# Kernel optimization log

Hardware: AMD Instinct MI355X
Metric: run time of the kernel (lower is better)

## Reference

```python
import jax, jax.numpy as jnp
import numpy as np

N_NODES = 50000
N_HYPEREDGES = 50000
E = 320000
D = 256


def _prelu(x, a):
    return jnp.where(x >= 0, x, a * x)


def _hypergraph_conv(x, hei, W, b, num_nodes, num_edges):
    # PyG HypergraphConv, use_attention=False, heads=1:
    # out = D^{-1} H B^{-1} H^T (X W^T) + b
    src = hei[0]  # node indices, [E]
    he = hei[1]   # hyperedge indices, [E]
    xw = x @ W.T  # [N, D] node transform (lin has no bias)
    ones = jnp.ones((hei.shape[1],), x.dtype)
    deg_n = jax.ops.segment_sum(ones, src, num_segments=num_nodes)   # node degree D
    deg_e = jax.ops.segment_sum(ones, he, num_segments=num_edges)    # hyperedge size B
    d_inv = jnp.where(deg_n > 0, 1.0 / deg_n, 0.0)
    b_inv = jnp.where(deg_e > 0, 1.0 / deg_e, 0.0)
    # node -> hyperedge aggregation, scaled by B^{-1}
    edge_feat = b_inv[:, None] * jax.ops.segment_sum(xw[src], he, num_segments=num_edges)  # [n_he, D]
    # hyperedge -> node aggregation, scaled by D^{-1}
    out = d_inv[:, None] * jax.ops.segment_sum(edge_feat[he], src, num_segments=num_nodes)  # [N, D]
    return out + b


def setup_inputs() -> dict:
    key = jax.random.key(0)
    ks = jax.random.split(key, 6)
    std = np.sqrt(2.0 / D)  # kaiming_normal
    x = jax.random.normal(ks[0], (N_NODES, D), dtype=jnp.float32)
    hyper_edge_index = jax.random.randint(ks[1], (2, E), 0, N_HYPEREDGES, dtype=jnp.int64)
    W1 = jax.random.normal(ks[2], (D, D), dtype=jnp.float32) * std
    b1 = jnp.zeros((D,), jnp.float32)
    W2 = jax.random.normal(ks[3], (D, D), dtype=jnp.float32) * std
    b2 = jnp.zeros((D,), jnp.float32)
    prelu_a = jnp.asarray(0.25, jnp.float32)
    return {"x": x, "W1": W1, "b1": b1, "W2": W2, "b2": b2,
            "prelu_a": prelu_a, "hyper_edge_index": hyper_edge_index}


def reference(x, W1, b1, W2, b2, prelu_a, hyper_edge_index):
    out = _hypergraph_conv(x, hyper_edge_index, W1, b1, N_NODES, N_HYPEREDGES)
    out = _prelu(out, prelu_a)
    out = _hypergraph_conv(out, hyper_edge_index, W2, b2, N_NODES, N_HYPEREDGES)
    out = out + x  # residual
    out = _prelu(out, prelu_a)
    return out
```

## Files before the change

### kernel.cpp

```cpp
#include <hip/hip_runtime.h>

#define NN    50000
#define NHE   50000
#define NEDGE 320000
#define DD    256

#define SB    1024
#define NBLK  ((NN + SB - 1) / SB)

typedef float f32x4 __attribute__((ext_vector_type(4)));
typedef short short8 __attribute__((ext_vector_type(8)));

static __device__ __forceinline__ unsigned short f2b(float f) {
    union { float f; unsigned u; } c; c.f = f;
    unsigned u = c.u;
    u += 0x7fffu + ((u >> 16) & 1u);
    return (unsigned short)(u >> 16);
}
static __device__ __forceinline__ float b2f_lo(unsigned v) {
    union { unsigned u; float f; } c; c.u = v << 16; return c.f;
}
static __device__ __forceinline__ float b2f_hi(unsigned v) {
    union { unsigned u; float f; } c; c.u = v & 0xffff0000u; return c.f;
}
static __device__ __forceinline__ unsigned pack2(float a, float b) {
    return (unsigned)f2b(a) | ((unsigned)f2b(b) << 16);
}

static __device__ __forceinline__ void glds16(const unsigned short* g, unsigned short* l) {
    __builtin_amdgcn_global_load_lds((const __attribute__((address_space(1))) unsigned int*)g,
                                     (__attribute__((address_space(3))) unsigned int*)l,
                                     16, 0, 0);
}

__global__ __launch_bounds__(256) void k_count(const int* __restrict__ src,
                                               const int* __restrict__ he,
                                               int* __restrict__ cnt_n,
                                               int* __restrict__ cnt_e,
                                               int* __restrict__ rank_n,
                                               int* __restrict__ rank_e) {
    int t  = blockIdx.x * 256 + threadIdx.x;
    int e0 = t * 4;
    if (e0 >= NEDGE) return;
    int4 s = *(const int4*)(src + e0);
    int4 h = *(const int4*)(he + e0);
    int4 rn, re;
    rn.x = atomicAdd(&cnt_n[s.x], 1);
    rn.y = atomicAdd(&cnt_n[s.y], 1);
    rn.z = atomicAdd(&cnt_n[s.z], 1);
    rn.w = atomicAdd(&cnt_n[s.w], 1);
    re.x = atomicAdd(&cnt_e[h.x], 1);
    re.y = atomicAdd(&cnt_e[h.y], 1);
    re.z = atomicAdd(&cnt_e[h.z], 1);
    re.w = atomicAdd(&cnt_e[h.w], 1);
    *(int4*)(rank_n + e0) = rn;
    *(int4*)(rank_e + e0) = re;
}

__global__ __launch_bounds__(256) void k_scan_a(const int* __restrict__ cnt_n,
                                                const int* __restrict__ cnt_e,
                                                int* __restrict__ bsum,
                                                const float* __restrict__ w1,
                                                const float* __restrict__ w2,
                                                unsigned short* __restrict__ o1,
                                                unsigned short* __restrict__ o2) {
    int b = blockIdx.x;
    if (b >= 2 * NBLK) {
        int t = (b - 2 * NBLK) * 256 + threadIdx.x;
        const int n4 = DD * DD / 4;
        const float* s = (t < n4) ? w1 : w2;
        unsigned short* d = (t < n4) ? o1 : o2;
        int i = (t < n4) ? t : t - n4;
        float4 v = ((const float4*)s)[i];
        uint2 o;
        o.x = pack2(v.x, v.y);
        o.y = pack2(v.z, v.w);
        ((uint2*)d)[i] = o;
        return;
    }
    int seg = b / NBLK, lb = b % NBLK;
    const int* cnt = seg ? cnt_e : cnt_n;
    int t = threadIdx.x;
    int idx = lb * SB + t * 4;
    int s = 0;
#pragma unroll
    for (int j = 0; j < 4; ++j)
        if (idx + j < NN) s += cnt[idx + j];
    __shared__ int red[256];
    red[t] = s;
    __syncthreads();
    for (int o = 128; o > 0; o >>= 1) {
        if (t < o) red[t] += red[t + o];
        __syncthreads();
    }
    if (t == 0) bsum[b] = red[0];
}

__global__ __launch_bounds__(64) void k_scan_b(const int* __restrict__ bsum,
                                               int* __restrict__ bbase) {
    if (threadIdx.x == 0) {
        int r = 0;
        for (int i = 0; i < NBLK; ++i) { bbase[i] = r; r += bsum[i]; }
        bbase[2 * NBLK] = r;
        r = 0;
        for (int i = NBLK; i < 2 * NBLK; ++i) { bbase[i] = r; r += bsum[i]; }
        bbase[2 * NBLK + 1] = r;
    }
}

__global__ __launch_bounds__(256) void k_scan_c(const int* __restrict__ cnt_n,
                                                const int* __restrict__ cnt_e,
                                                const int* __restrict__ bbase,
                                                int* __restrict__ off_n,
                                                int* __restrict__ off_e) {
    int b   = blockIdx.x;
    int seg = b / NBLK, lb = b % NBLK;
    const int* cnt = seg ? cnt_e : cnt_n;
    int* off = seg ? off_e : off_n;
    int t = threadIdx.x;
    int idx = lb * SB + t * 4;
    int v[4];
    int tsum = 0;
#pragma unroll
    for (int j = 0; j < 4; ++j) {
        v[j] = (idx + j < NN) ? cnt[idx + j] : 0;
        tsum += v[j];
    }
    __shared__ int sc[256];
    sc[t] = tsum;
    __syncthreads();
    for (int o = 1; o < 256; o <<= 1) {
        int val = (t >= o) ? sc[t - o] : 0;
        __syncthreads();
        sc[t] += val;
        __syncthreads();
    }
    int p = bbase[b] + sc[t] - tsum;
#pragma unroll
    for (int j = 0; j < 4; ++j) {
        if (idx + j < NN) off[idx + j] = p;
        p += v[j];
    }
    if (b == 0 && t == 0) off_n[NN] = bbase[2 * NBLK];
    if (b == NBLK && t == 0) off_e[NHE] = bbase[2 * NBLK + 1];
}

__global__ __launch_bounds__(256) void k_fill(const int* __restrict__ src,
                                              const int* __restrict__ he,
                                              const int* __restrict__ off_n,
                                              const int* __restrict__ off_e,
                                              const int* __restrict__ rank_n,
                                              const int* __restrict__ rank_e,
                                              int* __restrict__ adj_n,
                                              int* __restrict__ adj_e) {
    int t  = blockIdx.x * 256 + threadIdx.x;
    int e0 = t * 4;
    if (e0 >= NEDGE) return;
    int4 s  = *(const int4*)(src + e0);
    int4 h  = *(const int4*)(he + e0);
    int4 rn = *(const int4*)(rank_n + e0);
    int4 re = *(const int4*)(rank_e + e0);
    int on0 = off_n[s.x], on1 = off_n[s.y], on2 = off_n[s.z], on3 = off_n[s.w];
    int oe0 = off_e[h.x], oe1 = off_e[h.y], oe2 = off_e[h.z], oe3 = off_e[h.w];
    adj_n[on0 + rn.x] = h.x;
    adj_n[on1 + rn.y] = h.y;
    adj_n[on2 + rn.z] = h.z;
    adj_n[on3 + rn.w] = h.w;
    adj_e[oe0 + re.x] = s.x;
    adj_e[oe1 + re.y] = s.y;
    adj_e[oe2 + re.z] = s.z;
    adj_e[oe3 + re.w] = s.w;
}

template <bool A32>
__global__ __launch_bounds__(256) void k_gemm128(const void* __restrict__ Av,
                                                 const unsigned short* __restrict__ Wb,
                                                 unsigned short* __restrict__ Cb, int M) {
    __shared__ __align__(16) unsigned short As[128 * 32];
    __shared__ __align__(16) unsigned short Bs[128 * 32];
    const int t    = threadIdx.x;
    const int m0   = blockIdx.x * 128;
    const int n0   = blockIdx.y * 128;
    const int lane = t & 63;
    const int wave = t >> 6;
    const int wm   = (wave >> 1) * 64;
    const int wn   = (wave & 1) * 64;
    const int fr   = lane & 15;
    const int fq   = lane >> 4;

    f32x4 acc[4][4] = {};

    const int rl0 = wave * 32 + (lane >> 2);
    const int ar = t >> 1;
    const int ah = t & 1;

    for (int k0 = 0; k0 < DD; k0 += 32) {
        __syncthreads();
#pragma unroll
        for (int q = 0; q < 2; ++q) {
            int rl = rl0 + q * 16;
            int c  = (lane & 3) ^ (rl & 3);
            glds16(Wb + (size_t)(n0 + rl) * DD + k0 + c * 8,
                   Bs + (size_t)(wave * 32 + q * 16) * 32);
        }
        if (A32) {
            int gr = m0 + ar; if (gr >= M) gr = M - 1;
            const float* p = (const float*)Av + (size_t)gr * DD + k0 + ah * 16;
            float4 f0 = ((const float4*)p)[0];
            float4 f1 = ((const float4*)p)[1];
            float4 f2 = ((const float4*)p)[2];
            float4 f3 = ((const float4*)p)[3];
            uint4 u0, u1;
            u0.x = pack2(f0.x, f0.y); u0.y = pack2(f0.z, f0.w);
            u0.z = pack2(f1.x, f1.y); u0.w = pack2(f1.z, f1.w);
            u1.x = pack2(f2.x, f2.y); u1.y = pack2(f2.z, f2.w);
            u1.z = pack2(f3.x, f3.y); u1.w = pack2(f3.z, f3.w);
            int p0 = (2 * ah) ^ (ar & 3);
            int p1 = (2 * ah + 1) ^ (ar & 3);
            *(uint4*)(As + ar * 32 + p0 * 8) = u0;
            *(uint4*)(As + ar * 32 + p1 * 8) = u1;
        } else {
#pragma unroll
            for (int q = 0; q < 2; ++q) {
                int rl = rl0 + q * 16;
                int gr = m0 + rl; if (gr >= M) gr = M - 1;
                int c  = (lane & 3) ^ (rl & 3);
                glds16((const unsigned short*)Av + (size_t)gr * DD + k0 + c * 8,
                       As + (size_t)(wave * 32 + q * 16) * 32);
            }
        }
        __syncthreads();

        short8 af[4], bf[4];
#pragma unroll
        for (int mt = 0; mt < 4; ++mt) {
            int r = wm + mt * 16 + fr;
            af[mt] = *(const short8*)(As + r * 32 + ((fq ^ (r & 3)) * 8));
        }
#pragma unroll
        for (int nt = 0; nt < 4; ++nt) {
            int r = wn + nt * 16 + fr;
            bf[nt] = *(const short8*)(Bs + r * 32 + ((fq ^ (r & 3)) * 8));
        }
#pragma unroll
        for (int mt = 0; mt < 4; ++mt)
#pragma unroll
            for (int nt = 0; nt < 4; ++nt)
                acc[mt][nt] = __builtin_amdgcn_mfma_f32_16x16x32_bf16(af[mt], bf[nt],
                                                                      acc[mt][nt], 0, 0, 0);
    }

#pragma unroll
    for (int mt = 0; mt < 4; ++mt) {
#pragma unroll
        for (int i = 0; i < 4; ++i) {
            int gm = m0 + wm + mt * 16 + fq * 4 + i;
            if (gm >= M) continue;
#pragma unroll
            for (int nt = 0; nt < 4; ++nt) {
                int gn = n0 + wn + nt * 16 + fr;
                Cb[(size_t)gm * DD + gn] = f2b(acc[mt][nt][i]);
            }
        }
    }
}

static __device__ __forceinline__ void acc8(float* a, uint4 v) {
    a[0] += b2f_lo(v.x); a[1] += b2f_hi(v.x);
    a[2] += b2f_lo(v.y); a[3] += b2f_hi(v.y);
    a[4] += b2f_lo(v.z); a[5] += b2f_hi(v.z);
    a[6] += b2f_lo(v.w); a[7] += b2f_hi(v.w);
}
static __device__ __forceinline__ void gather8(const unsigned short* __restrict__ srcb,
                                               const int* __restrict__ adj,
                                               int b, int e, int sl, float* a) {
#pragma unroll
    for (int i = 0; i < 8; ++i) a[i] = 0.f;
    for (int i = b; i < e; i += 8) {
        int g0 = adj[i];
        int g[8];
        g[0] = g0;
#pragma unroll
        for (int j = 1; j < 8; ++j) g[j] = (i + j < e) ? adj[i + j] : g0;
        uint4 v[8];
#pragma unroll
        for (int j = 0; j < 8; ++j)
            v[j] = *(const uint4*)(srcb + (size_t)g[j] * DD + sl * 8);
        acc8(a, v[0]);
#pragma unroll
        for (int j = 1; j < 8; ++j)
            if (i + j < e) acc8(a, v[j]);
    }
}

__global__ __launch_bounds__(256) void k_gather_edge_b(const unsigned short* __restrict__ xw,
                                                       unsigned short* __restrict__ ef,
                                                       const int* __restrict__ off,
                                                       const int* __restrict__ adj) {
    int tid = blockIdx.x * 256 + threadIdx.x;
    int w = tid >> 5;
    int sl = tid & 31;
    if (w >= NHE) return;
    int b = off[w], e = off[w + 1];
    float a[8];
    gather8(xw, adj, b, e, sl, a);
    float sc = (e > b) ? 1.f / (float)(e - b) : 0.f;
    uint4 o;
    o.x = pack2(a[0] * sc, a[1] * sc);
    o.y = pack2(a[2] * sc, a[3] * sc);
    o.z = pack2(a[4] * sc, a[5] * sc);
    o.w = pack2(a[6] * sc, a[7] * sc);
    *(uint4*)(ef + (size_t)w * DD + sl * 8) = o;
}

__global__ __launch_bounds__(256) void k_gather_node_mid_b(const unsigned short* __restrict__ ef,
                                                           unsigned short* __restrict__ h,
                                                           const int* __restrict__ off,
                                                           const int* __restrict__ adj,
                                                           const float* __restrict__ bias,
                                                           const float* __restrict__ aP) {
    int tid = blockIdx.x * 256 + threadIdx.x;
    int w = tid >> 5;
    int sl = tid & 31;
    if (w >= NN) return;
    int b = off[w], e = off[w + 1];
    float a[8];
    gather8(ef, adj, b, e, sl, a);
    float sc = (e > b) ? 1.f / (float)(e - b) : 0.f;
    float al = *aP;
    float4 bb0 = ((const float4*)bias)[sl * 2];
    float4 bb1 = ((const float4*)bias)[sl * 2 + 1];
    float r[8];
    r[0] = a[0] * sc + bb0.x; r[1] = a[1] * sc + bb0.y;
    r[2] = a[2] * sc + bb0.z; r[3] = a[3] * sc + bb0.w;
    r[4] = a[4] * sc + bb1.x; r[5] = a[5] * sc + bb1.y;
    r[6] = a[6] * sc + bb1.z; r[7] = a[7] * sc + bb1.w;
#pragma unroll
    for (int i = 0; i < 8; ++i) r[i] = (r[i] >= 0.f) ? r[i] : al * r[i];
    uint4 o;
    o.x = pack2(r[0], r[1]);
    o.y = pack2(r[2], r[3]);
    o.z = pack2(r[4], r[5]);
    o.w = pack2(r[6], r[7]);
    *(uint4*)(h + (size_t)w * DD + sl * 8) = o;
}

__global__ __launch_bounds__(256) void k_gather_node_final_b(const unsigned short* __restrict__ ef,
                                                             const float* __restrict__ x,
                                                             float* __restrict__ out,
                                                             const int* __restrict__ off,
                                                             const int* __restrict__ adj,
                                                             const float* __restrict__ bias,
                                                             const float* __restrict__ aP) {
    int tid = blockIdx.x * 256 + threadIdx.x;
    int w = tid >> 5;
    int sl = tid & 31;
    if (w >= NN) return;
    int b = off[w], e = off[w + 1];
    float a[8];
    gather8(ef, adj, b, e, sl, a);
    float sc = (e > b) ? 1.f / (float)(e - b) : 0.f;
    float al = *aP;
    float4 bb0 = ((const float4*)bias)[sl * 2];
    float4 bb1 = ((const float4*)bias)[sl * 2 + 1];
    const float* xp = x + (size_t)w * DD + sl * 8;
    float4 xv0 = *(const float4*)xp;
    float4 xv1 = *(const float4*)(xp + 4);
    float r[8];
    r[0] = a[0] * sc + bb0.x + xv0.x; r[1] = a[1] * sc + bb0.y + xv0.y;
    r[2] = a[2] * sc + bb0.z + xv0.z; r[3] = a[3] * sc + bb0.w + xv0.w;
    r[4] = a[4] * sc + bb1.x + xv1.x; r[5] = a[5] * sc + bb1.y + xv1.y;
    r[6] = a[6] * sc + bb1.z + xv1.z; r[7] = a[7] * sc + bb1.w + xv1.w;
#pragma unroll
    for (int i = 0; i < 8; ++i) r[i] = (r[i] >= 0.f) ? r[i] : al * r[i];
    float* op = out + (size_t)w * DD + sl * 8;
    *(float4*)op = make_float4(r[0], r[1], r[2], r[3]);
    *(float4*)(op + 4) = make_float4(r[4], r[5], r[6], r[7]);
}

extern "C" void kernel_launch(void* const* d_in, const int* in_sizes, int n_in,
                              void* d_out, int out_size, void* d_ws, size_t ws_size,
                              hipStream_t stream) {
    const float* x       = (const float*)d_in[0];
    const float* W1      = (const float*)d_in[1];
    const float* b1      = (const float*)d_in[2];
    const float* W2      = (const float*)d_in[3];
    const float* b2      = (const float*)d_in[4];
    const float* prelu_a = (const float*)d_in[5];
    const int*   hei     = (const int*)d_in[6];
    const int* idx_src = hei;
    const int* idx_he  = hei + NEDGE;

    float* out = (float*)d_out;
    unsigned short* B1 = (unsigned short*)d_ws;
    unsigned short* B2 = B1 + (size_t)NN * DD;
    int* off_n  = (int*)(B2 + (size_t)NN * DD);
    int* off_e  = off_n + NN + 1;
    int* cnt_n  = off_e + NHE + 1;
    int* cnt_e  = cnt_n + NN;
    int* adj_n  = cnt_e + NHE;
    int* adj_e  = adj_n + NEDGE;
    int* rank_n = adj_e + NEDGE;
    int* rank_e = rank_n + NEDGE;
    int* bsum   = rank_e + NEDGE;
    int* bbase  = bsum + 2 * NBLK;
    unsigned short* w1b = (unsigned short*)d_out;
    unsigned short* w2b = w1b + DD * DD;

    const int e4blocks = (NEDGE / 4 + 255) / 256;
    const int gblocks = (NN * 32 + 255) / 256;
    dim3 ggrid((NN + 127) / 128, DD / 128);

    hipMemsetAsync(cnt_n, 0, sizeof(int) * (NN + NHE), stream);
    k_count<<<e4blocks, 256, 0, stream>>>(idx_src, idx_he, cnt_n, cnt_e,
                                          rank_n, rank_e);
    k_scan_a<<<2 * NBLK + 128, 256, 0, stream>>>(cnt_n, cnt_e, bsum,
                                                 W1, W2, w1b, w2b);
    k_scan_b<<<1, 64, 0, stream>>>(bsum, bbase);
    k_scan_c<<<2 * NBLK, 256, 0, stream>>>(cnt_n, cnt_e, bbase, off_n, off_e);
    k_fill<<<e4blocks, 256, 0, stream>>>(idx_src, idx_he, off_n, off_e,
                                         rank_n, rank_e, adj_n, adj_e);

    k_gemm128<true><<<ggrid, 256, 0, stream>>>((const void*)x, w1b, B1, NN);
    k_gather_edge_b<<<gblocks, 256, 0, stream>>>(B1, B2, off_e, adj_e);
    k_gather_node_mid_b<<<gblocks, 256, 0, stream>>>(B2, B1, off_n, adj_n, b1, prelu_a);

    k_gemm128<false><<<ggrid, 256, 0, stream>>>((const void*)B1, w2b, B2, NN);
    k_gather_edge_b<<<gblocks, 256, 0, stream>>>(B2, B1, off_e, adj_e);
    k_gather_node_final_b<<<gblocks, 256, 0, stream>>>(B1, x, out, off_n, adj_n, b2, prelu_a);
}
```

Measured before the change: 308.9 us.

## Merge setup kernels, fold scan_b into scan_c, remap gathers to two rows per wave

Moves the weight bf16 conversion into the count kernel and drops the single-thread scan_b kernel by having each scan_c block compute its own base from the block sums. Runs the CSR fill and the first GEMM as one launch through block-index dispatch. Changes the gather kernels so each 64-lane wave processes two rows with 8-byte loads per lane and interleaved neighbor fetches, instead of one row per 32 lanes with 16-byte loads. This cuts launch count and serial gaps. The fused fill+GEMM has no dependency between its parts, but the per-block serial prefix and the narrower loads may add cost.

```diff
diff --git a/kernel.cpp b/kernel.cpp
--- a/kernel.cpp
+++ b/kernel.cpp
@@ -7,6 +7,7 @@
 
 #define SB    1024
 #define NBLK  ((NN + SB - 1) / SB)
+#define CNTB  ((NEDGE / 4 + 255) / 256)
 
 typedef float f32x4 __attribute__((ext_vector_type(4)));
 typedef short short8 __attribute__((ext_vector_type(8)));
@@ -33,13 +34,31 @@
                                      16, 0, 0);
 }
 
-__global__ __launch_bounds__(256) void k_count(const int* __restrict__ src,
-                                               const int* __restrict__ he,
-                                               int* __restrict__ cnt_n,
-                                               int* __restrict__ cnt_e,
-                                               int* __restrict__ rank_n,
-                                               int* __restrict__ rank_e) {
-    int t  = blockIdx.x * 256 + threadIdx.x;
+__global__ __launch_bounds__(256) void k_count_cvt(const int* __restrict__ src,
+                                                   const int* __restrict__ he,
+                                                   int* __restrict__ cnt_n,
+                                                   int* __restrict__ cnt_e,
+                                                   int* __restrict__ rank_n,
+                                                   int* __restrict__ rank_e,
+                                                   const float* __restrict__ w1,
+                                                   const float* __restrict__ w2,
+                                                   unsigned short* __restrict__ o1,
+                                                   unsigned short* __restrict__ o2) {
+    int bx = blockIdx.x;
+    if (bx >= CNTB) {
+        int t = (bx - CNTB) * 256 + threadIdx.x;
+        const int n4 = DD * DD / 4;
+        const float* s = (t < n4) ? w1 : w2;
+        unsigned short* d = (t < n4) ? o1 : o2;
+        int i = (t < n4) ? t : t - n4;
+        float4 v = ((const float4*)s)[i];
+        uint2 o;
+        o.x = pack2(v.x, v.y);
+        o.y = pack2(v.z, v.w);
+        ((uint2*)d)[i] = o;
+        return;
+    }
+    int t  = bx * 256 + threadIdx.x;
     int e0 = t * 4;
     if (e0 >= NEDGE) return;
     int4 s = *(const int4*)(src + e0);
@@ -59,25 +78,8 @@
 
 __global__ __launch_bounds__(256) void k_scan_a(const int* __restrict__ cnt_n,
                                                 const int* __restrict__ cnt_e,
-                                                int* __restrict__ bsum,
-                                                const float* __restrict__ w1,
-                                                const float* __restrict__ w2,
-                                                unsigned short* __restrict__ o1,
-                                                unsigned short* __restrict__ o2) {
-    int b = blockIdx.x;
-    if (b >= 2 * NBLK) {
-        int t = (b - 2 * NBLK) * 256 + threadIdx.x;
-        const int n4 = DD * DD / 4;
-        const float* s = (t < n4) ? w1 : w2;
-        unsigned short* d = (t < n4) ? o1 : o2;
-        int i = (t < n4) ? t : t - n4;
-        float4 v = ((const float4*)s)[i];
-        uint2 o;
-        o.x = pack2(v.x, v.y);
-        o.y = pack2(v.z, v.w);
-        ((uint2*)d)[i] = o;
-        return;
-    }
+                                                int* __restrict__ bsum) {
+    int b   = blockIdx.x;
     int seg = b / NBLK, lb = b % NBLK;
     const int* cnt = seg ? cnt_e : cnt_n;
     int t = threadIdx.x;
@@ -96,21 +98,9 @@
     if (t == 0) bsum[b] = red[0];
 }
 
-__global__ __launch_bounds__(64) void k_scan_b(const int* __restrict__ bsum,
-                                               int* __restrict__ bbase) {
-    if (threadIdx.x == 0) {
-        int r = 0;
-        for (int i = 0; i < NBLK; ++i) { bbase[i] = r; r += bsum[i]; }
-        bbase[2 * NBLK] = r;
-        r = 0;
-        for (int i = NBLK; i < 2 * NBLK; ++i) { bbase[i] = r; r += bsum[i]; }
-        bbase[2 * NBLK + 1] = r;
-    }
-}
-
 __global__ __launch_bounds__(256) void k_scan_c(const int* __restrict__ cnt_n,
                                                 const int* __restrict__ cnt_e,
-                                                const int* __restrict__ bbase,
+                                                const int* __restrict__ bsum,
                                                 int* __restrict__ off_n,
                                                 int* __restrict__ off_e) {
     int b   = blockIdx.x;
@@ -118,6 +108,15 @@
     const int* cnt = seg ? cnt_e : cnt_n;
     int* off = seg ? off_e : off_n;
     int t = threadIdx.x;
+    __shared__ int sb[NBLK];
+    __shared__ int binfo[2];
+    if (t < NBLK) sb[t] = bsum[seg * NBLK + t];
+    __syncthreads();
+    if (t == 0) {
+        int base = 0, tot = 0;
+        for (int j = 0; j < NBLK; ++j) { if (j < lb) base += sb[j]; tot += sb[j]; }
+        binfo[0] = base; binfo[1] = tot;
+    }
     int idx = lb * SB + t * 4;
     int v[4];
     int tsum = 0;
@@ -135,52 +134,24 @@
         sc[t] += val;
         __syncthreads();
     }
-    int p = bbase[b] + sc[t] - tsum;
+    int p = binfo[0] + sc[t] - tsum;
 #pragma unroll
     for (int j = 0; j < 4; ++j) {
         if (idx + j < NN) off[idx + j] = p;
         p += v[j];
     }
-    if (b == 0 && t == 0) off_n[NN] = bbase[2 * NBLK];
-    if (b == NBLK && t == 0) off_e[NHE] = bbase[2 * NBLK + 1];
-}
-
-__global__ __launch_bounds__(256) void k_fill(const int* __restrict__ src,
-                                              const int* __restrict__ he,
-                                              const int* __restrict__ off_n,
-                                              const int* __restrict__ off_e,
-                                              const int* __restrict__ rank_n,
-                                              const int* __restrict__ rank_e,
-                                              int* __restrict__ adj_n,
-                                              int* __restrict__ adj_e) {
-    int t  = blockIdx.x * 256 + threadIdx.x;
-    int e0 = t * 4;
-    if (e0 >= NEDGE) return;
-    int4 s  = *(const int4*)(src + e0);
-    int4 h  = *(const int4*)(he + e0);
-    int4 rn = *(const int4*)(rank_n + e0);
-    int4 re = *(const int4*)(rank_e + e0);
-    int on0 = off_n[s.x], on1 = off_n[s.y], on2 = off_n[s.z], on3 = off_n[s.w];
-    int oe0 = off_e[h.x], oe1 = off_e[h.y], oe2 = off_e[h.z], oe3 = off_e[h.w];
-    adj_n[on0 + rn.x] = h.x;
-    adj_n[on1 + rn.y] = h.y;
-    adj_n[on2 + rn.z] = h.z;
-    adj_n[on3 + rn.w] = h.w;
-    adj_e[oe0 + re.x] = s.x;
-    adj_e[oe1 + re.y] = s.y;
-    adj_e[oe2 + re.z] = s.z;
-    adj_e[oe3 + re.w] = s.w;
+    if (b == 0 && t == 0) off_n[NN] = binfo[1];
+    if (b == NBLK && t == 0) off_e[NHE] = binfo[1];
 }
 
 template <bool A32>
-__global__ __launch_bounds__(256) void k_gemm128(const void* __restrict__ Av,
-                                                 const unsigned short* __restrict__ Wb,
-                                                 unsigned short* __restrict__ Cb, int M) {
+static __device__ __forceinline__ void gemm128_body(const void* __restrict__ Av,
+                                                    const unsigned short* __restrict__ Wb,
+                                                    unsigned short* __restrict__ Cb,
+                                                    int M, int m0, int n0) {
     __shared__ __align__(16) unsigned short As[128 * 32];
     __shared__ __align__(16) unsigned short Bs[128 * 32];
     const int t    = threadIdx.x;
-    const int m0   = blockIdx.x * 128;
-    const int n0   = blockIdx.y * 128;
     const int lane = t & 63;
     const int wave = t >> 6;
     const int wm   = (wave >> 1) * 64;
@@ -265,117 +236,187 @@
     }
 }
 
-static __device__ __forceinline__ void acc8(float* a, uint4 v) {
+__global__ __launch_bounds__(256) void k_fill_gemm1(const int* __restrict__ src,
+                                                    const int* __restrict__ he,
+                                                    const int* __restrict__ off_n,
+                                                    const int* __restrict__ off_e,
+                                                    const int* __restrict__ rank_n,
+                                                    const int* __restrict__ rank_e,
+                                                    int* __restrict__ adj_n,
+                                                    int* __restrict__ adj_e,
+                                                    const float* __restrict__ x,
+                                                    const unsigned short* __restrict__ w1b,
+                                                    unsigned short* __restrict__ B1) {
+    int bx = blockIdx.x;
+    if (bx < CNTB) {
+        int t  = bx * 256 + threadIdx.x;
+        int e0 = t * 4;
+        if (e0 >= NEDGE) return;
+        int4 s  = *(const int4*)(src + e0);
+        int4 h  = *(const int4*)(he + e0);
+        int4 rn = *(const int4*)(rank_n + e0);
+        int4 re = *(const int4*)(rank_e + e0);
+        int on0 = off_n[s.x], on1 = off_n[s.y], on2 = off_n[s.z], on3 = off_n[s.w];
+        int oe0 = off_e[h.x], oe1 = off_e[h.y], oe2 = off_e[h.z], oe3 = off_e[h.w];
+        adj_n[on0 + rn.x] = h.x;
+        adj_n[on1 + rn.y] = h.y;
+        adj_n[on2 + rn.z] = h.z;
+        adj_n[on3 + rn.w] = h.w;
+        adj_e[oe0 + re.x] = s.x;
+        adj_e[oe1 + re.y] = s.y;
+        adj_e[oe2 + re.z] = s.z;
+        adj_e[oe3 + re.w] = s.w;
+        return;
+    }
+    int id = bx - CNTB;
+    int nt = id & 1, mt = id >> 1;
+    gemm128_body<true>((const void*)x, w1b, B1, NN, mt * 128, nt * 128);
+}
+
+__global__ __launch_bounds__(256) void k_gemm2(const unsigned short* __restrict__ Av,
+                                               const unsigned short* __restrict__ Wb,
+                                               unsigned short* __restrict__ Cb) {
+    gemm128_body<false>((const void*)Av, Wb, Cb, NN, blockIdx.y * 128, blockIdx.x * 128);
+}
+
+static __device__ __forceinline__ void acc4(float* a, uint2 v) {
     a[0] += b2f_lo(v.x); a[1] += b2f_hi(v.x);
     a[2] += b2f_lo(v.y); a[3] += b2f_hi(v.y);
-    a[4] += b2f_lo(v.z); a[5] += b2f_hi(v.z);
-    a[6] += b2f_lo(v.w); a[7] += b2f_hi(v.w);
-}
-static __device__ __forceinline__ void gather8(const unsigned short* __restrict__ srcb,
+}
+static __device__ __forceinline__ void gather2(const unsigned short* __restrict__ srcb,
                                                const int* __restrict__ adj,
-                                               int b, int e, int sl, float* a) {
-#pragma unroll
-    for (int i = 0; i < 8; ++i) a[i] = 0.f;
-    for (int i = b; i < e; i += 8) {
-        int g0 = adj[i];
-        int g[8];
-        g[0] = g0;
-#pragma unroll
-        for (int j = 1; j < 8; ++j) g[j] = (i + j < e) ? adj[i + j] : g0;
-        uint4 v[8];
-#pragma unroll
-        for (int j = 0; j < 8; ++j)
-            v[j] = *(const uint4*)(srcb + (size_t)g[j] * DD + sl * 8);
-        acc8(a, v[0]);
-#pragma unroll
-        for (int j = 1; j < 8; ++j)
-            if (i + j < e) acc8(a, v[j]);
-    }
-}
-
-__global__ __launch_bounds__(256) void k_gather_edge_b(const unsigned short* __restrict__ xw,
-                                                       unsigned short* __restrict__ ef,
-                                                       const int* __restrict__ off,
-                                                       const int* __restrict__ adj) {
+                                               int b0, int e0, int b1, int e1,
+                                               int ln, float* a0, float* a1) {
+#pragma unroll
+    for (int i = 0; i < 4; ++i) { a0[i] = 0.f; a1[i] = 0.f; }
+    int i0 = b0, i1 = b1;
+    while (i0 < e0 || i1 < e1) {
+        uint2 v0[8], v1[8];
+        bool act0 = i0 < e0, act1 = i1 < e1;
+        if (act0) {
+            int gg = adj[i0];
+            int g[8];
+            g[0] = gg;
+#pragma unroll
+            for (int j = 1; j < 8; ++j) g[j] = (i0 + j < e0) ? adj[i0 + j] : gg;
+#pragma unroll
+            for (int j = 0; j < 8; ++j)
+                v0[j] = *(const uint2*)(srcb + (size_t)g[j] * DD + ln * 4);
+        }
+        if (act1) {
+            int gg = adj[i1];
+            int g[8];
+            g[0] = gg;
+#pragma unroll
+            for (int j = 1; j < 8; ++j) g[j] = (i1 + j < e1) ? adj[i1 + j] : gg;
+#pragma unroll
+            for (int j = 0; j < 8; ++j)
+                v1[j] = *(const uint2*)(srcb + (size_t)g[j] * DD + ln * 4);
+        }
+        if (act0) {
+            acc4(a0, v0[0]);
+#pragma unroll
+            for (int j = 1; j < 8; ++j)
+                if (i0 + j < e0) acc4(a0, v0[j]);
+        }
+        if (act1) {
+            acc4(a1, v1[0]);
+#pragma unroll
+            for (int j = 1; j < 8; ++j)
+                if (i1 + j < e1) acc4(a1, v1[j]);
+        }
+        i0 += 8; i1 += 8;
+    }
+}
+
+__global__ __launch_bounds__(256) void k_gather_edge2(const unsigned short* __restrict__ xw,
+                                                      unsigned short* __restrict__ ef,
+                                                      const int* __restrict__ off,
+                                                      const int* __restrict__ adj) {
     int tid = blockIdx.x * 256 + threadIdx.x;
-    int w = tid >> 5;
-    int sl = tid & 31;
-    if (w >= NHE) return;
-    int b = off[w], e = off[w + 1];
-    float a[8];
-    gather8(xw, adj, b, e, sl, a);
-    float sc = (e > b) ? 1.f / (float)(e - b) : 0.f;
-    uint4 o;
-    o.x = pack2(a[0] * sc, a[1] * sc);
-    o.y = pack2(a[2] * sc, a[3] * sc);
-    o.z = pack2(a[4] * sc, a[5] * sc);
-    o.w = pack2(a[6] * sc, a[7] * sc);
-    *(uint4*)(ef + (size_t)w * DD + sl * 8) = o;
-}
-
-__global__ __launch_bounds__(256) void k_gather_node_mid_b(const unsigned short* __restrict__ ef,
-                                                           unsigned short* __restrict__ h,
-                                                           const int* __restrict__ off,
-                                                           const int* __restrict__ adj,
-                                                           const float* __restrict__ bias,
-                                                           const float* __restrict__ aP) {
+    int wv = tid >> 6;
+    int ln = tid & 63;
+    int r0 = wv * 2, r1 = r0 + 1;
+    if (r0 >= NHE) return;
+    int b0 = off[r0], e0 = off[r0 + 1];
+    int b1 = off[r1], e1 = off[r1 + 1];
+    float a0[4], a1[4];
+    gather2(xw, adj, b0, e0, b1, e1, ln, a0, a1);
+    float s0 = (e0 > b0) ? 1.f / (float)(e0 - b0) : 0.f;
+    float s1 = (e1 > b1) ? 1.f / (float)(e1 - b1) : 0.f;
+    uint2 o0, o1;
+    o0.x = pack2(a0[0] * s0, a0[1] * s0);
+    o0.y = pack2(a0[2] * s0, a0[3] * s0);
+    o1.x = pack2(a1[0] * s1, a1[1] * s1);
+    o1.y = pack2(a1[2] * s1, a1[3] * s1);
+    *(uint2*)(ef + (size_t)r0 * DD + ln * 4) = o0;
+    *(uint2*)(ef + (size_t)r1 * DD + ln * 4) = o1;
+}
+
+__global__ __launch_bounds__(256) void k_gather_node_mid2(const unsigned short* __restrict__ ef,
+                                                          unsigned short* __restrict__ h,
+                                                          const int* __restrict__ off,
+                                                          const int* __restrict__ adj,
+                                                          const float* __restrict__ bias,
+                                                          const float* __restrict__ aP) {
     int tid = blockIdx.x * 256 + threadIdx.x;
-    int w = tid >> 5;
-    int sl = tid & 31;
-    if (w >= NN) return;
-    int b = off[w], e = off[w + 1];
-    float a[8];
-    gather8(ef, adj, b, e, sl, a);
-    float sc = (e > b) ? 1.f / (float)(e - b) : 0.f;
+    int wv = tid >> 6;
+    int ln = tid & 63;
+    int r0 = wv * 2, r1 = r0 + 1;
+    if (r0 >= NN) return;
+    int b0 = off[r0], e0 = off[r0 + 1];
+    int b1 = off[r1], e1 = off[r1 + 1];
+    float a0[4], a1[4];
+    gather2(ef, adj, b0, e0, b1, e1, ln, a0, a1);
+    float s0 = (e0 > b0) ? 1.f / (float)(e0 - b0) : 0.f;
+    float s1 = (e1 > b1) ? 1.f / (float)(e1 - b1) : 0.f;
     float al = *aP;
-    float4 bb0 = ((const float4*)bias)[sl * 2];
-    float4 bb1 = ((const float4*)bias)[sl * 2 + 1];
+    float4 bb = ((const float4*)bias)[ln];
     float r[8];
-    r[0] = a[0] * sc + bb0.x; r[1] = a[1] * sc + bb0.y;
-    r[2] = a[2] * sc + bb0.z; r[3] = a[3] * sc + bb0.w;
-    r[4] = a[4] * sc + bb1.x; r[5] = a[5] * sc + bb1.y;
-    r[6] = a[6] * sc + bb1.z; r[7] = a[7] * sc + bb1.w;
+    r[0] = a0[0] * s0 + bb.x; r[1] = a0[1] * s0 + bb.y;
+    r[2] = a0[2] * s0 + bb.z; r[3] = a0[3] * s0 + bb.w;
+    r[4] = a1[0] * s1 + bb.x; r[5] = a1[1] * s1 + bb.y;
+    r[6] = a1[2] * s1 + bb.z; r[7] = a1[3] * s1 + bb.w;
 #pragma unroll
     for (int i = 0; i < 8; ++i) r[i] = (r[i] >= 0.f) ? r[i] : al * r[i];
-    uint4 o;
-    o.x = pack2(r[0], r[1]);
-    o.y = pack2(r[2], r[3]);
-    o.z = pack2(r[4], r[5]);
-    o.w = pack2(r[6], r[7]);
-    *(uint4*)(h + (size_t)w * DD + sl * 8) = o;
-}
-
-__global__ __launch_bounds__(256) void k_gather_node_final_b(const unsigned short* __restrict__ ef,
-                                                             const float* __restrict__ x,
-                                                             float* __restrict__ out,
-                                                             const int* __restrict__ off,
-                                                             const int* __restrict__ adj,
-                                                             const float* __restrict__ bias,
-                                                             const float* __restrict__ aP) {
+    uint2 o0, o1;
+    o0.x = pack2(r[0], r[1]); o0.y = pack2(r[2], r[3]);
+    o1.x = pack2(r[4], r[5]); o1.y = pack2(r[6], r[7]);
+    *(uint2*)(h + (size_t)r0 * DD + ln * 4) = o0;
+    *(uint2*)(h + (size_t)r1 * DD + ln * 4) = o1;
+}
+
+__global__ __launch_bounds__(256) void k_gather_node_final2(const unsigned short* __restrict__ ef,
+                                                            const float* __restrict__ x,
+                                                            float* __restrict__ out,
+                                                            const int* __restrict__ off,
+                                                            const int* __restrict__ adj,
+                                                            const float* __restrict__ bias,
+                                                            const float* __restrict__ aP) {
     int tid = blockIdx.x * 256 + threadIdx.x;
-    int w = tid >> 5;
-    int sl = tid & 31;
-    if (w >= NN) return;
-    int b = off[w], e = off[w + 1];
-    float a[8];
-    gather8(ef, adj, b, e, sl, a);
-    float sc = (e > b) ? 1.f / (float)(e - b) : 0.f;
+    int wv = tid >> 6;
+    int ln = tid & 63;
+    int r0 = wv * 2, r1 = r0 + 1;
+    if (r0 >= NN) return;
+    int b0 = off[r0], e0 = off[r0 + 1];
+    int b1 = off[r1], e1 = off[r1 + 1];
+    float a0[4], a1[4];
+    gather2(ef, adj, b0, e0, b1, e1, ln, a0, a1);
+    float s0 = (e0 > b0) ? 1.f / (float)(e0 - b0) : 0.f;
+    float s1 = (e1 > b1) ? 1.f / (float)(e1 - b1) : 0.f;
     float al = *aP;
-    float4 bb0 = ((const float4*)bias)[sl * 2];
-    float4 bb1 = ((const float4*)bias)[sl * 2 + 1];
-    const float* xp = x + (size_t)w * DD + sl * 8;
-    float4 xv0 = *(const float4*)xp;
-    float4 xv1 = *(const float4*)(xp + 4);
+    float4 bb = ((const float4*)bias)[ln];
+    float4 xv0 = *(const float4*)(x + (size_t)r0 * DD + ln * 4);
+    float4 xv1 = *(const float4*)(x + (size_t)r1 * DD + ln * 4);
     float r[8];
-    r[0] = a[0] * sc + bb0.x + xv0.x; r[1] = a[1] * sc + bb0.y + xv0.y;
-    r[2] = a[2] * sc + bb0.z + xv0.z; r[3] = a[3] * sc + bb0.w + xv0.w;
-    r[4] = a[4] * sc + bb1.x + xv1.x; r[5] = a[5] * sc + bb1.y + xv1.y;
-    r[6] = a[6] * sc + bb1.z + xv1.z; r[7] = a[7] * sc + bb1.w + xv1.w;
+    r[0] = a0[0] * s0 + bb.x + xv0.x; r[1] = a0[1] * s0 + bb.y + xv0.y;
+    r[2] = a0[2] * s0 + bb.z + xv0.z; r[3] = a0[3] * s0 + bb.w + xv0.w;
+    r[4] = a1[0] * s1 + bb.x + xv1.x; r[5] = a1[1] * s1 + bb.y + xv1.y;
+    r[6] = a1[2] * s1 + bb.z + xv1.z; r[7] = a1[3] * s1 + bb.w + xv1.w;
 #pragma unroll
     for (int i = 0; i < 8; ++i) r[i] = (r[i] >= 0.f) ? r[i] : al * r[i];
-    float* op = out + (size_t)w * DD + sl * 8;
-    *(float4*)op = make_float4(r[0], r[1], r[2], r[3]);
-    *(float4*)(op + 4) = make_float4(r[4], r[5], r[6], r[7]);
+    *(float4*)(out + (size_t)r0 * DD + ln * 4) = make_float4(r[0], r[1], r[2], r[3]);
+    *(float4*)(out + (size_t)r1 * DD + ln * 4) = make_float4(r[4], r[5], r[6], r[7]);
 }
 
 extern "C" void kernel_launch(void* const* d_in, const int* in_sizes, int n_in,
@@ -403,29 +444,25 @@
     int* rank_n = adj_e + NEDGE;
     int* rank_e = rank_n + NEDGE;
     int* bsum   = rank_e + NEDGE;
-    int* bbase  = bsum + 2 * NBLK;
     unsigned short* w1b = (unsigned short*)d_out;
     unsigned short* w2b = w1b + DD * DD;
 
-    const int e4blocks = (NEDGE / 4 + 255) / 256;
-    const int gblocks = (NN * 32 + 255) / 256;
-    dim3 ggrid((NN + 127) / 128, DD / 128);
+    const int gblocks = (NN / 2 * 64 + 255) / 256;
+    dim3 g2(DD / 128, (NN + 127) / 128);
 
     hipMemsetAsync(cnt_n, 0, sizeof(int) * (NN + NHE), stream);
-    k_count<<<e4blocks, 256, 0, stream>>>(idx_src, idx_he, cnt_n, cnt_e,
-                                          rank_n, rank_e);
-    k_scan_a<<<2 * NBLK + 128, 256, 0, stream>>>(cnt_n, cnt_e, bsum,
-                                                 W1, W2, w1b, w2b);
-    k_scan_b<<<1, 64, 0, stream>>>(bsum, bbase);
-    k_scan_c<<<2 * NBLK, 256, 0, stream>>>(cnt_n, cnt_e, bbase, off_n, off_e);
-    k_fill<<<e4blocks, 256, 0, stream>>>(idx_src, idx_he, off_n, off_e,
-                                         rank_n, rank_e, adj_n, adj_e);
-
-    k_gemm128<true><<<ggrid, 256, 0, stream>>>((const void*)x, w1b, B1, NN);
-    k_gather_edge_b<<<gblocks, 256, 0, stream>>>(B1, B2, off_e, adj_e);
-    k_gather_node_mid_b<<<gblocks, 256, 0, stream>>>(B2, B1, off_n, adj_n, b1, prelu_a);
-
-    k_gemm128<false><<<ggrid, 256, 0, stream>>>((const void*)B1, w2b, B2, NN);
-    k_gather_edge_b<<<gblocks, 256, 0, stream>>>(B2, B1, off_e, adj_e);
-    k_gather_node_final_b<<<gblocks, 256, 0, stream>>>(B1, x, out, off_n, adj_n, b2, prelu_a);
-}
+    k_count_cvt<<<CNTB + 128, 256, 0, stream>>>(idx_src, idx_he, cnt_n, cnt_e,
+                                                rank_n, rank_e, W1, W2, w1b, w2b);
+    k_scan_a<<<2 * NBLK, 256, 0, stream>>>(cnt_n, cnt_e, bsum);
+    k_scan_c<<<2 * NBLK, 256, 0, stream>>>(cnt_n, cnt_e, bsum, off_n, off_e);
+
+    k_fill_gemm1<<<CNTB + 2 * ((NN + 127) / 128), 256, 0, stream>>>(
+        idx_src, idx_he, off_n, off_e, rank_n, rank_e, adj_n, adj_e,
+        x, w1b, B1);
+    k_gather_edge2<<<gblocks, 256, 0, stream>>>(B1, B2, off_e, adj_e);
+    k_gather_node_mid2<<<gblocks, 256, 0, stream>>>(B2, B1, off_n, adj_n, b1, prelu_a);
+
+    k_gemm2<<<g2, 256, 0, stream>>>(B1, w2b, B2);
+    k_gather_edge2<<<gblocks, 256, 0, stream>>>(B2, B1, off_e, adj_e);
+    k_gather_node_final2<<<gblocks, 256, 0, stream>>>(B1, x, out, off_n, adj_n, b2, prelu_a);
+}
```

Measured after the change: 314.1 us. About the same (+1.7%).

## Replace LDS-tiled GEMM with direct-load MFMA and trim scan kernels

Applied to the files above, without the earlier changes.

The GEMM no longer stages tiles through LDS with barriers. Each block now computes 64 rows by the full 256 columns, and MFMA fragments are loaded straight from global memory, relying on L2/L1 to serve the shared B weights. The weight bf16 conversion moves into the count kernel. The single-thread scan_b kernel is removed: each scan_c block recomputes its base from the block sums in LDS. This cuts kernel launches and barrier overhead, but it risks lower global-load efficiency and redundant weight reads per block.

```diff
diff --git a/kernel.cpp b/kernel.cpp
--- a/kernel.cpp
+++ b/kernel.cpp
@@ -7,6 +7,7 @@
 
 #define SB    1024
 #define NBLK  ((NN + SB - 1) / SB)
+#define CNTB  ((NEDGE / 4 + 255) / 256)
 
 typedef float f32x4 __attribute__((ext_vector_type(4)));
 typedef short short8 __attribute__((ext_vector_type(8)));
@@ -27,19 +28,31 @@
     return (unsigned)f2b(a) | ((unsigned)f2b(b) << 16);
 }
 
-static __device__ __forceinline__ void glds16(const unsigned short* g, unsigned short* l) {
-    __builtin_amdgcn_global_load_lds((const __attribute__((address_space(1))) unsigned int*)g,
-                                     (__attribute__((address_space(3))) unsigned int*)l,
-                                     16, 0, 0);
-}
-
-__global__ __launch_bounds__(256) void k_count(const int* __restrict__ src,
-                                               const int* __restrict__ he,
-                                               int* __restrict__ cnt_n,
-                                               int* __restrict__ cnt_e,
-                                               int* __restrict__ rank_n,
-                                               int* __restrict__ rank_e) {
-    int t  = blockIdx.x * 256 + threadIdx.x;
+__global__ __launch_bounds__(256) void k_count_cvt(const int* __restrict__ src,
+                                                   const int* __restrict__ he,
+                                                   int* __restrict__ cnt_n,
+                                                   int* __restrict__ cnt_e,
+                                                   int* __restrict__ rank_n,
+                                                   int* __restrict__ rank_e,
+                                                   const float* __restrict__ w1,
+                                                   const float* __restrict__ w2,
+                                                   unsigned short* __restrict__ o1,
+                                                   unsigned short* __restrict__ o2) {
+    int bx = blockIdx.x;
+    if (bx >= CNTB) {
+        int t = (bx - CNTB) * 256 + threadIdx.x;
+        const int n4 = DD * DD / 4;
+        const float* s = (t < n4) ? w1 : w2;
+        unsigned short* d = (t < n4) ? o1 : o2;
+        int i = (t < n4) ? t : t - n4;
+        float4 v = ((const float4*)s)[i];
+        uint2 o;
+        o.x = pack2(v.x, v.y);
+        o.y = pack2(v.z, v.w);
+        ((uint2*)d)[i] = o;
+        return;
+    }
+    int t  = bx * 256 + threadIdx.x;
     int e0 = t * 4;
     if (e0 >= NEDGE) return;
     int4 s = *(const int4*)(src + e0);
@@ -59,25 +72,8 @@
 
 __global__ __launch_bounds__(256) void k_scan_a(const int* __restrict__ cnt_n,
                                                 const int* __restrict__ cnt_e,
-                                                int* __restrict__ bsum,
-                                                const float* __restrict__ w1,
-                                                const float* __restrict__ w2,
-                                                unsigned short* __restrict__ o1,
-                                                unsigned short* __restrict__ o2) {
-    int b = blockIdx.x;
-    if (b >= 2 * NBLK) {
-        int t = (b - 2 * NBLK) * 256 + threadIdx.x;
-        const int n4 = DD * DD / 4;
-        const float* s = (t < n4) ? w1 : w2;
-        unsigned short* d = (t < n4) ? o1 : o2;
-        int i = (t < n4) ? t : t - n4;
-        float4 v = ((const float4*)s)[i];
-        uint2 o;
-        o.x = pack2(v.x, v.y);
-        o.y = pack2(v.z, v.w);
-        ((uint2*)d)[i] = o;
-        return;
-    }
+                                                int* __restrict__ bsum) {
+    int b   = blockIdx.x;
     int seg = b / NBLK, lb = b % NBLK;
     const int* cnt = seg ? cnt_e : cnt_n;
     int t = threadIdx.x;
@@ -96,21 +92,9 @@
     if (t == 0) bsum[b] = red[0];
 }
 
-__global__ __launch_bounds__(64) void k_scan_b(const int* __restrict__ bsum,
-                                               int* __restrict__ bbase) {
-    if (threadIdx.x == 0) {
-        int r = 0;
-        for (int i = 0; i < NBLK; ++i) { bbase[i] = r; r += bsum[i]; }
-        bbase[2 * NBLK] = r;
-        r = 0;
-        for (int i = NBLK; i < 2 * NBLK; ++i) { bbase[i] = r; r += bsum[i]; }
-        bbase[2 * NBLK + 1] = r;
-    }
-}
-
 __global__ __launch_bounds__(256) void k_scan_c(const int* __restrict__ cnt_n,
                                                 const int* __restrict__ cnt_e,
-                                                const int* __restrict__ bbase,
+                                                const int* __restrict__ bsum,
                                                 int* __restrict__ off_n,
                                                 int* __restrict__ off_e) {
     int b   = blockIdx.x;
@@ -118,6 +102,15 @@
     const int* cnt = seg ? cnt_e : cnt_n;
     int* off = seg ? off_e : off_n;
     int t = threadIdx.x;
+    __shared__ int sb[NBLK];
+    __shared__ int binfo[2];
+    if (t < NBLK) sb[t] = bsum[seg * NBLK + t];
+    __syncthreads();
+    if (t == 0) {
+        int base = 0, tot = 0;
+        for (int j = 0; j < NBLK; ++j) { if (j < lb) base += sb[j]; tot += sb[j]; }
+        binfo[0] = base; binfo[1] = tot;
+    }
     int idx = lb * SB + t * 4;
     int v[4];
     int tsum = 0;
@@ -135,14 +128,14 @@
         sc[t] += val;
         __syncthreads();
     }
-    int p = bbase[b] + sc[t] - tsum;
+    int p = binfo[0] + sc[t] - tsum;
 #pragma unroll
     for (int j = 0; j < 4; ++j) {
         if (idx + j < NN) off[idx + j] = p;
         p += v[j];
     }
-    if (b == 0 && t == 0) off_n[NN] = bbase[2 * NBLK];
-    if (b == NBLK && t == 0) off_e[NHE] = bbase[2 * NBLK + 1];
+    if (b == 0 && t == 0) off_n[NN] = binfo[1];
+    if (b == NBLK && t == 0) off_e[NHE] = binfo[1];
 }
 
 __global__ __launch_bounds__(256) void k_fill(const int* __restrict__ src,
@@ -173,96 +166,76 @@
 }
 
 template <bool A32>
-__global__ __launch_bounds__(256) void k_gemm128(const void* __restrict__ Av,
-                                                 const unsigned short* __restrict__ Wb,
-                                                 unsigned short* __restrict__ Cb, int M) {
-    __shared__ __align__(16) unsigned short As[128 * 32];
-    __shared__ __align__(16) unsigned short Bs[128 * 32];
+static __device__ __forceinline__ void gemm_direct(const void* __restrict__ Av,
+                                                   const unsigned short* __restrict__ Wb,
+                                                   unsigned short* __restrict__ Cb,
+                                                   int M, int m0) {
     const int t    = threadIdx.x;
-    const int m0   = blockIdx.x * 128;
-    const int n0   = blockIdx.y * 128;
     const int lane = t & 63;
     const int wave = t >> 6;
-    const int wm   = (wave >> 1) * 64;
-    const int wn   = (wave & 1) * 64;
+    const int wm   = (wave >> 1) * 32;
+    const int wn   = (wave & 1) * 128;
     const int fr   = lane & 15;
     const int fq   = lane >> 4;
 
-    f32x4 acc[4][4] = {};
-
-    const int rl0 = wave * 32 + (lane >> 2);
-    const int ar = t >> 1;
-    const int ah = t & 1;
-
+    f32x4 acc[2][8] = {};
+
+    int arow0 = m0 + wm + fr;      if (arow0 >= M) arow0 = M - 1;
+    int arow1 = m0 + wm + 16 + fr; if (arow1 >= M) arow1 = M - 1;
+
+#pragma unroll
     for (int k0 = 0; k0 < DD; k0 += 32) {
-        __syncthreads();
-#pragma unroll
-        for (int q = 0; q < 2; ++q) {
-            int rl = rl0 + q * 16;
-            int c  = (lane & 3) ^ (rl & 3);
-            glds16(Wb + (size_t)(n0 + rl) * DD + k0 + c * 8,
-                   Bs + (size_t)(wave * 32 + q * 16) * 32);
+        short8 af[2], bf[8];
+        if (A32) {
+            const float* p0 = (const float*)Av + (size_t)arow0 * DD + k0 + fq * 8;
+            const float* p1 = (const float*)Av + (size_t)arow1 * DD + k0 + fq * 8;
+            float4 a0 = ((const float4*)p0)[0];
+            float4 a1 = ((const float4*)p0)[1];
+            float4 a2 = ((const float4*)p1)[0];
+            float4 a3 = ((const float4*)p1)[1];
+            uint4 u0, u1;
+            u0.x = pack2(a0.x, a0.y); u0.y = pack2(a0.z, a0.w);
+            u0.z = pack2(a1.x, a1.y); u0.w = pack2(a1.z, a1.w);
+            u1.x = pack2(a2.x, a2.y); u1.y = pack2(a2.z, a2.w);
+            u1.z = pack2(a3.x, a3.y); u1.w = pack2(a3.z, a3.w);
+            af[0] = *(short8*)&u0;
+            af[1] = *(short8*)&u1;
+        } else {
+            af[0] = *(const short8*)((const unsigned short*)Av + (size_t)arow0 * DD + k0 + fq * 8);
+            af[1] = *(const short8*)((const unsigned short*)Av + (size_t)arow1 * DD + k0 + fq * 8);
         }
-        if (A32) {
-            int gr = m0 + ar; if (gr >= M) gr = M - 1;
-            const float* p = (const float*)Av + (size_t)gr * DD + k0 + ah * 16;
-            float4 f0 = ((const float4*)p)[0];
-            float4 f1 = ((const float4*)p)[1];
-            float4 f2 = ((const float4*)p)[2];
-            float4 f3 = ((const float4*)p)[3];
-            uint4 u0, u1;
-            u0.x = pack2(f0.x, f0.y); u0.y = pack2(f0.z, f0.w);
-            u0.z = pack2(f1.x, f1.y); u0.w = pack2(f1.z, f1.w);
-            u1.x = pack2(f2.x, f2.y); u1.y = pack2(f2.z, f2.w);
-            u1.z = pack2(f3.x, f3.y); u1.w = pack2(f3.z, f3.w);
-            int p0 = (2 * ah) ^ (ar & 3);
-            int p1 = (2 * ah + 1) ^ (ar & 3);
-            *(uint4*)(As + ar * 32 + p0 * 8) = u0;
-            *(uint4*)(As + ar * 32 + p1 * 8) = u1;
-        } else {
-#pragma unroll
-            for (int q = 0; q < 2; ++q) {
-                int rl = rl0 + q * 16;
-                int gr = m0 + rl; if (gr >= M) gr = M - 1;
-                int c  = (lane & 3) ^ (rl & 3);
-                glds16((const unsigned short*)Av + (size_t)gr * DD + k0 + c * 8,
-                       As + (size_t)(wave * 32 + q * 16) * 32);
-            }
-        }
-        __syncthreads();
-
-        short8 af[4], bf[4];
-#pragma unroll
-        for (int mt = 0; mt < 4; ++mt) {
-            int r = wm + mt * 16 + fr;
-            af[mt] = *(const short8*)(As + r * 32 + ((fq ^ (r & 3)) * 8));
-        }
-#pragma unroll
-        for (int nt = 0; nt < 4; ++nt) {
-            int r = wn + nt * 16 + fr;
-            bf[nt] = *(const short8*)(Bs + r * 32 + ((fq ^ (r & 3)) * 8));
-        }
-#pragma unroll
-        for (int mt = 0; mt < 4; ++mt)
-#pragma unroll
-            for (int nt = 0; nt < 4; ++nt)
+#pragma unroll
+        for (int nt = 0; nt < 8; ++nt)
+            bf[nt] = *(const short8*)(Wb + (size_t)(wn + nt * 16 + fr) * DD + k0 + fq * 8);
+#pragma unroll
+        for (int mt = 0; mt < 2; ++mt)
+#pragma unroll
+            for (int nt = 0; nt < 8; ++nt)
                 acc[mt][nt] = __builtin_amdgcn_mfma_f32_16x16x32_bf16(af[mt], bf[nt],
                                                                       acc[mt][nt], 0, 0, 0);
     }
 
 #pragma unroll
-    for (int mt = 0; mt < 4; ++mt) {
+    for (int mt = 0; mt < 2; ++mt)
 #pragma unroll
         for (int i = 0; i < 4; ++i) {
             int gm = m0 + wm + mt * 16 + fq * 4 + i;
             if (gm >= M) continue;
 #pragma unroll
-            for (int nt = 0; nt < 4; ++nt) {
-                int gn = n0 + wn + nt * 16 + fr;
-                Cb[(size_t)gm * DD + gn] = f2b(acc[mt][nt][i]);
-            }
+            for (int nt = 0; nt < 8; ++nt)
+                Cb[(size_t)gm * DD + wn + nt * 16 + fr] = f2b(acc[mt][nt][i]);
         }
-    }
+}
+
+__global__ __launch_bounds__(256) void k_gemm1(const float* __restrict__ x,
+                                               const unsigned short* __restrict__ Wb,
+                                               unsigned short* __restrict__ Cb) {
+    gemm_direct<true>((const void*)x, Wb, Cb, NN, blockIdx.x * 64);
+}
+__global__ __launch_bounds__(256) void k_gemm2(const unsigned short* __restrict__ Av,
+                                               const unsigned short* __restrict__ Wb,
+                                               unsigned short* __restrict__ Cb) {
+    gemm_direct<false>((const void*)Av, Wb, Cb, NN, blockIdx.x * 64);
 }
 
 static __device__ __forceinline__ void acc8(float* a, uint4 v) {
@@ -403,29 +376,25 @@
     int* rank_n = adj_e + NEDGE;
     int* rank_e = rank_n + NEDGE;
     int* bsum   = rank_e + NEDGE;
-    int* bbase  = bsum + 2 * NBLK;
     unsigned short* w1b = (unsigned short*)d_out;
     unsigned short* w2b = w1b + DD * DD;
 
-    const int e4blocks = (NEDGE / 4 + 255) / 256;
     const int gblocks = (NN * 32 + 255) / 256;
-    dim3 ggrid((NN + 127) / 128, DD / 128);
+    const int mblocks = (NN + 63) / 64;
 
     hipMemsetAsync(cnt_n, 0, sizeof(int) * (NN + NHE), stream);
-    k_count<<<e4blocks, 256, 0, stream>>>(idx_src, idx_he, cnt_n, cnt_e,
-                                          rank_n, rank_e);
-    k_scan_a<<<2 * NBLK + 128, 256, 0, stream>>>(cnt_n, cnt_e, bsum,
-                                                 W1, W2, w1b, w2b);
-    k_scan_b<<<1, 64, 0, stream>>>(bsum, bbase);
-    k_scan_c<<<2 * NBLK, 256, 0, stream>>>(cnt_n, cnt_e, bbase, off_n, off_e);
-    k_fill<<<e4blocks, 256, 0, stream>>>(idx_src, idx_he, off_n, off_e,
-                                         rank_n, rank_e, adj_n, adj_e);
-
-    k_gemm128<true><<<ggrid, 256, 0, stream>>>((const void*)x, w1b, B1, NN);
+    k_count_cvt<<<CNTB + 128, 256, 0, stream>>>(idx_src, idx_he, cnt_n, cnt_e,
+                                                rank_n, rank_e, W1, W2, w1b, w2b);
+    k_scan_a<<<2 * NBLK, 256, 0, stream>>>(cnt_n, cnt_e, bsum);
+    k_scan_c<<<2 * NBLK, 256, 0, stream>>>(cnt_n, cnt_e, bsum, off_n, off_e);
+    k_fill<<<CNTB, 256, 0, stream>>>(idx_src, idx_he, off_n, off_e,
+                                     rank_n, rank_e, adj_n, adj_e);
+
+    k_gemm1<<<mblocks, 256, 0, stream>>>(x, w1b, B1);
     k_gather_edge_b<<<gblocks, 256, 0, stream>>>(B1, B2, off_e, adj_e);
     k_gather_node_mid_b<<<gblocks, 256, 0, stream>>>(B2, B1, off_n, adj_n, b1, prelu_a);
 
-    k_gemm128<false><<<ggrid, 256, 0, stream>>>((const void*)B1, w2b, B2, NN);
+    k_gemm2<<<mblocks, 256, 0, stream>>>(B1, w2b, B2);
     k_gather_edge_b<<<gblocks, 256, 0, stream>>>(B2, B1, off_e, adj_e);
     k_gather_node_final_b<<<gblocks, 256, 0, stream>>>(B1, x, out, off_n, adj_n, b2, prelu_a);
 }
```

Result: slower. 351.2 us (+13.7%).
